# Optimization experiments

Hardware: AMD Instinct MI355X
Metric: run time of the kernel (lower is better)

The kernel has to match this reference:

```python
import jax, jax.numpy as jnp
import numpy as np

N, E, D, L, V = 200000, 500000, 128, 5, 8
BN_EPS = 1e-5


def _bn(h, g, b, m, v):
    # eval-mode BatchNorm1d with running stats
    return (h - m) * jax.lax.rsqrt(v + BN_EPS) * g + b


def setup_inputs() -> dict:
    key = jax.random.key(0)
    ks = iter(jax.random.split(key, 40))
    nk = lambda: next(ks)
    f = lambda shape: jax.random.normal(nk(), shape, jnp.float32) * 0.05
    inp = {}
    inp["x"] = jax.random.normal(nk(), (N, 12), jnp.float32)
    inp["edge_index"] = jax.random.randint(nk(), (2, E), 0, N, dtype=jnp.int32)
    inp["edge_attr"] = jax.random.randint(nk(), (E, 3), 0, V, dtype=jnp.int32)
    # atom encoder: Lin(12,D) -> BN -> ReLU -> Lin(D,D) -> BN -> ReLU -> Lin(D,D)
    inp["ae_W1"] = f((12, D)); inp["ae_b1"] = jnp.zeros((D,), jnp.float32)
    inp["ae_g1"] = jnp.ones((D,), jnp.float32); inp["ae_be1"] = jnp.zeros((D,), jnp.float32)
    inp["ae_m1"] = f((D,)); inp["ae_v1"] = jax.random.uniform(nk(), (D,), jnp.float32) + 0.5
    inp["ae_W2"] = f((D, D)); inp["ae_b2"] = jnp.zeros((D,), jnp.float32)
    inp["ae_g2"] = jnp.ones((D,), jnp.float32); inp["ae_be2"] = jnp.zeros((D,), jnp.float32)
    inp["ae_m2"] = f((D,)); inp["ae_v2"] = jax.random.uniform(nk(), (D,), jnp.float32) + 0.5
    inp["ae_W3"] = f((D, D)); inp["ae_b3"] = jnp.zeros((D,), jnp.float32)
    # per-layer GIN params (stacked over L)
    inp["bond_emb"] = f((L, 3, V, D))
    inp["eps"] = jnp.zeros((L,), jnp.float32)
    inp["mlp_W1"] = f((L, D, D)); inp["mlp_b1"] = jnp.zeros((L, D), jnp.float32)
    inp["mlp_g"] = jnp.ones((L, D), jnp.float32); inp["mlp_be"] = jnp.zeros((L, D), jnp.float32)
    inp["mlp_m"] = f((L, D)); inp["mlp_v"] = jax.random.uniform(nk(), (L, D), jnp.float32) + 0.5
    inp["mlp_W2"] = f((L, D, D)); inp["mlp_b2"] = jnp.zeros((L, D), jnp.float32)
    # per-layer outer BatchNorm
    inp["out_g"] = jnp.ones((L, D), jnp.float32); inp["out_be"] = jnp.zeros((L, D), jnp.float32)
    inp["out_m"] = f((L, D)); inp["out_v"] = jax.random.uniform(nk(), (L, D), jnp.float32) + 0.5
    return inp


def reference(x, edge_index, edge_attr,
              ae_W1, ae_b1, ae_g1, ae_be1, ae_m1, ae_v1,
              ae_W2, ae_b2, ae_g2, ae_be2, ae_m2, ae_v2,
              ae_W3, ae_b3,
              bond_emb, eps, mlp_W1, mlp_b1, mlp_g, mlp_be, mlp_m, mlp_v,
              mlp_W2, mlp_b2, out_g, out_be, out_m, out_v):
    n_nodes = x.shape[0]
    src, dst = edge_index[0], edge_index[1]
    # atom encoder
    h = jax.nn.relu(_bn(x @ ae_W1 + ae_b1, ae_g1, ae_be1, ae_m1, ae_v1))
    h = jax.nn.relu(_bn(h @ ae_W2 + ae_b2, ae_g2, ae_be2, ae_m2, ae_v2))
    h = h @ ae_W3 + ae_b3  # [N, D]
    n_layers = bond_emb.shape[0]
    for l in range(n_layers):
        # BondEncoder: sum of per-feature embeddings -> [E, D]
        be = bond_emb[l]
        e_emb = be[0][edge_attr[:, 0]] + be[1][edge_attr[:, 1]] + be[2][edge_attr[:, 2]]
        # message: relu(x_j + edge_emb); aggregate: scatter-add at dst
        msg = jax.nn.relu(h[src] + e_emb)
        agg = jax.ops.segment_sum(msg, dst, num_segments=n_nodes)
        z = (1.0 + eps[l]) * h + agg
        # GIN MLP: Lin -> BN -> ReLU -> Lin
        z = jax.nn.relu(_bn(z @ mlp_W1[l] + mlp_b1[l], mlp_g[l], mlp_be[l], mlp_m[l], mlp_v[l]))
        z = z @ mlp_W2[l] + mlp_b2[l]
        # outer BatchNorm; ReLU on all but last layer (dropout is identity in eval)
        z = _bn(z, out_g[l], out_be[l], out_m[l], out_v[l])
        if l < n_layers - 1:
            z = jax.nn.relu(z)
        h = z
    return h  # JK='last'
```

## Files before the change

### kernel.cpp

```cpp
#include <hip/hip_runtime.h>
#include <hip/hip_bf16.h>
#include <cstdint>
#include <cstddef>

#define D 128
#define NNODES 200000
#define NEDGES 500000
#define NLAYERS 5
#define BN_EPS 1e-5f
#define MAXDEG 24

typedef __attribute__((ext_vector_type(8))) short bf16x8;
typedef __attribute__((ext_vector_type(4))) float f32x4;

__device__ __forceinline__ unsigned short f2bf(float f) {
    union { float f; unsigned int u; } x; x.f = f;
    unsigned int r = (x.u + 0x7FFFu + ((x.u >> 16) & 1u)) >> 16;
    return (unsigned short)r;
}
__device__ __forceinline__ float bf2f(unsigned short u) {
    union { unsigned int u; float f; } x; x.u = ((unsigned int)u) << 16; return x.f;
}

__global__ void k_zero(int* __restrict__ p, int n) {
    int i = blockIdx.x * 256 + threadIdx.x;
    if (i < n) p[i] = 0;
}

__global__ void k_fill_edges(const int* __restrict__ ei, const int* __restrict__ ea,
                             int* __restrict__ deg, int* __restrict__ elist, int n_edges) {
    int e = blockIdx.x * 256 + threadIdx.x;
    if (e >= n_edges) return;
    int dst = ei[n_edges + e];
    int src = ei[e];
    int a0 = ea[e * 3], a1 = ea[e * 3 + 1], a2 = ea[e * 3 + 2];
    int rec = src | (a0 << 18) | (a1 << 21) | (a2 << 24);
    int pos = atomicAdd(&deg[dst], 1);
    if (pos < MAXDEG) elist[dst * MAXDEG + pos] = rec;
}

__global__ void k_prep_w(const float* __restrict__ aeW2, const float* __restrict__ aeW3,
                         const float* __restrict__ mlpW1, const float* __restrict__ mlpW2,
                         unsigned short* __restrict__ wbt) {
    int m = blockIdx.x >> 3;
    int s = (blockIdx.x & 7) * 256 + threadIdx.x;
    int f = s >> 4;
    int kc = (s & 15) * 8;
    const float* W;
    if (m == 0) W = aeW2;
    else if (m == 1) W = aeW3;
    else if (m < 7) W = mlpW1 + (size_t)(m - 2) * D * D;
    else W = mlpW2 + (size_t)(m - 7) * D * D;
    unsigned short tmp[8];
#pragma unroll
    for (int j = 0; j < 8; ++j) tmp[j] = f2bf(W[(size_t)(kc + j) * D + f]);
    *(int4*)(wbt + (size_t)m * D * D + (size_t)f * D + kc) = *(int4*)tmp;
}

__global__ void k_bondsum(const float* __restrict__ bond, float* __restrict__ bsum) {
    int idx = blockIdx.x;
    int l = idx >> 9, combo = idx & 511;
    int a0 = combo & 7, a1 = (combo >> 3) & 7, a2 = (combo >> 6) & 7;
    int f = threadIdx.x;
    const float* bl = bond + (size_t)l * 3 * 8 * 128;
    bsum[(size_t)idx * 128 + f] =
        bl[a0 * 128 + f] + bl[1024 + a1 * 128 + f] + bl[2048 + a2 * 128 + f];
}

__global__ void k_ae1(const float* __restrict__ x, const float* __restrict__ W,
                      const float* __restrict__ b, const float* __restrict__ g,
                      const float* __restrict__ be, const float* __restrict__ m,
                      const float* __restrict__ v, unsigned short* __restrict__ out) {
    __shared__ float sW[12][128];
    int tid = threadIdx.x;
    for (int i = tid; i < 12 * 128; i += 256) sW[i >> 7][i & 127] = W[i];
    int f0 = (tid & 31) * 4;
    int g8 = tid >> 5;
    float4 bb = *(const float4*)(b + f0);
    float4 gg = *(const float4*)(g + f0);
    float4 ee = *(const float4*)(be + f0);
    float4 mm = *(const float4*)(m + f0);
    float4 vv = *(const float4*)(v + f0);
    float A0 = gg.x * rsqrtf(vv.x + BN_EPS), S0 = (bb.x - mm.x) * A0 + ee.x;
    float A1 = gg.y * rsqrtf(vv.y + BN_EPS), S1 = (bb.y - mm.y) * A1 + ee.y;
    float A2 = gg.z * rsqrtf(vv.z + BN_EPS), S2 = (bb.z - mm.z) * A2 + ee.z;
    float A3 = gg.w * rsqrtf(vv.w + BN_EPS), S3 = (bb.w - mm.w) * A3 + ee.w;
    __syncthreads();
    for (int n = blockIdx.x * 8 + g8; n < NNODES; n += gridDim.x * 8) {
        const float4* xr = (const float4*)(x + (size_t)n * 12);
        float4 x0 = xr[0], x1 = xr[1], x2 = xr[2];
        float xv[12] = {x0.x, x0.y, x0.z, x0.w, x1.x, x1.y, x1.z, x1.w,
                        x2.x, x2.y, x2.z, x2.w};
        float a0 = 0.f, a1 = 0.f, a2 = 0.f, a3 = 0.f;
#pragma unroll
        for (int k = 0; k < 12; ++k) {
            float4 wv = *(float4*)&sW[k][f0];
            a0 += xv[k] * wv.x; a1 += xv[k] * wv.y;
            a2 += xv[k] * wv.z; a3 += xv[k] * wv.w;
        }
        unsigned short o[4];
        o[0] = f2bf(fmaxf(a0 * A0 + S0, 0.f));
        o[1] = f2bf(fmaxf(a1 * A1 + S1, 0.f));
        o[2] = f2bf(fmaxf(a2 * A2 + S2, 0.f));
        o[3] = f2bf(fmaxf(a3 * A3 + S3, 0.f));
        *(uint2*)(out + (size_t)n * D + f0) = *(uint2*)o;
    }
}

__launch_bounds__(256, 7)
__global__ void k_agg(const unsigned short* __restrict__ hin,
                      const float* __restrict__ bsum,
                      const float* __restrict__ eps_arr, int layer,
                      const int* __restrict__ deg, const int* __restrict__ elist,
                      unsigned short* __restrict__ out) {
    int tid = threadIdx.x;
    int f4 = tid & 31;
    int n = blockIdx.x * 8 + (tid >> 5);
    int dgr = min(deg[n], MAXDEG);
    int rec = (f4 < MAXDEG) ? elist[(size_t)n * MAXDEG + f4] : 0;
    float epsv = 1.f + eps_arr[layer];
    ushort4 hs = *(const ushort4*)(hin + (size_t)n * D + f4 * 4);
    float z0 = epsv * bf2f(hs.x), z1 = epsv * bf2f(hs.y);
    float z2 = epsv * bf2f(hs.z), z3 = epsv * bf2f(hs.w);

    ushort4 hv[6]; float4 bv[6]; int rr[6];
#pragma unroll
    for (int j = 0; j < 6; ++j) {
        rr[j] = __shfl(rec, j, 32);
        if (j < dgr) {
            hv[j] = *(const ushort4*)(hin + (size_t)(rr[j] & 0x3FFFF) * D + f4 * 4);
            bv[j] = *(const float4*)(bsum + (size_t)((rr[j] >> 18) & 511) * D + f4 * 4);
        }
    }
#pragma unroll
    for (int j = 0; j < 6; ++j) {
        if (j < dgr) {
            z0 += fmaxf(bf2f(hv[j].x) + bv[j].x, 0.f);
            z1 += fmaxf(bf2f(hv[j].y) + bv[j].y, 0.f);
            z2 += fmaxf(bf2f(hv[j].z) + bv[j].z, 0.f);
            z3 += fmaxf(bf2f(hv[j].w) + bv[j].w, 0.f);
        }
    }
    for (int base = 6; base < dgr; base += 4) {
        ushort4 hw[4]; float4 bw[4]; int rt[4];
#pragma unroll
        for (int j = 0; j < 4; ++j) {
            rt[j] = __shfl(rec, base + j, 32);
            if (base + j < dgr) {
                hw[j] = *(const ushort4*)(hin + (size_t)(rt[j] & 0x3FFFF) * D + f4 * 4);
                bw[j] = *(const float4*)(bsum + (size_t)((rt[j] >> 18) & 511) * D + f4 * 4);
            }
        }
#pragma unroll
        for (int j = 0; j < 4; ++j) {
            if (base + j < dgr) {
                z0 += fmaxf(bf2f(hw[j].x) + bw[j].x, 0.f);
                z1 += fmaxf(bf2f(hw[j].y) + bw[j].y, 0.f);
                z2 += fmaxf(bf2f(hw[j].z) + bw[j].z, 0.f);
                z3 += fmaxf(bf2f(hw[j].w) + bw[j].w, 0.f);
            }
        }
    }
    unsigned short o[4] = {f2bf(z0), f2bf(z1), f2bf(z2), f2bf(z3)};
    *(uint2*)(out + (size_t)n * D + f4 * 4) = *(uint2*)o;
}

#define SWZ(row, bytecol) (((row) * 256 + (bytecol)) ^ (((row) & 7) << 4))
template<int OUTF32>
__launch_bounds__(512, 6)
__global__ void k_mlp2(const unsigned short* __restrict__ hin,
                       const unsigned short* __restrict__ W1t,
                       const float* __restrict__ b1,
                       const float* __restrict__ g1, const float* __restrict__ be1,
                       const float* __restrict__ m1, const float* __restrict__ v1,
                       const unsigned short* __restrict__ W2t,
                       const float* __restrict__ b2,
                       const float* __restrict__ g2, const float* __restrict__ be2,
                       const float* __restrict__ m2, const float* __restrict__ v2,
                       unsigned short* __restrict__ outb, float* __restrict__ outf,
                       int do_bn2, int do_relu2) {
    __shared__ char sA[16384];
    int tid = threadIdx.x;
    size_t nb = (size_t)blockIdx.x * 64;
    int lane = tid & 63;
    int w = tid >> 6;
    int arow = lane & 15;
    int kq = (lane >> 4) * 8;
    int c = w * 16 + arow;

    bf16x8 w1f[4], w2f[4];
#pragma unroll
    for (int kb = 0; kb < 4; ++kb) {
        w1f[kb] = *(const bf16x8*)(W1t + (size_t)c * D + kb * 32 + kq);
        w2f[kb] = *(const bf16x8*)(W2t + (size_t)c * D + kb * 32 + kq);
    }
#pragma unroll
    for (int i = 0; i < 2; ++i) {
        int s = tid + i * 512;
        int r = s >> 4, cc = (s & 15) * 16;
        *(int4*)(sA + SWZ(r, cc)) = *(const int4*)((const char*)hin + (nb + r) * 256 + cc);
    }
    __syncthreads();

    f32x4 acc[4];
#pragma unroll
    for (int rt = 0; rt < 4; ++rt) acc[rt] = (f32x4){0.f, 0.f, 0.f, 0.f};
#pragma unroll
    for (int kb = 0; kb < 4; ++kb) {
        int k0 = kb * 32 + kq;
#pragma unroll
        for (int rt = 0; rt < 4; ++rt) {
            bf16x8 a = *(bf16x8*)(sA + SWZ(rt * 16 + arow, k0 * 2));
            acc[rt] = __builtin_amdgcn_mfma_f32_16x16x32_bf16(a, w1f[kb], acc[rt], 0, 0, 0);
        }
    }
    __syncthreads();

    {
        float sc = g1[c] * rsqrtf(v1[c] + BN_EPS);
        float sh = (b1[c] - m1[c]) * sc + be1[c];
#pragma unroll
        for (int rt = 0; rt < 4; ++rt) {
#pragma unroll
            for (int r = 0; r < 4; ++r) {
                int row = rt * 16 + (lane >> 4) * 4 + r;
                float z = fmaxf(acc[rt][r] * sc + sh, 0.f);
                *(unsigned short*)(sA + SWZ(row, c * 2)) = f2bf(z);
            }
        }
    }
    __syncthreads();

#pragma unroll
    for (int rt = 0; rt < 4; ++rt) acc[rt] = (f32x4){0.f, 0.f, 0.f, 0.f};
#pragma unroll
    for (int kb = 0; kb < 4; ++kb) {
        int k0 = kb * 32 + kq;
#pragma unroll
        for (int rt = 0; rt < 4; ++rt) {
            bf16x8 a = *(bf16x8*)(sA + SWZ(rt * 16 + arow, k0 * 2));
            acc[rt] = __builtin_amdgcn_mfma_f32_16x16x32_bf16(a, w2f[kb], acc[rt], 0, 0, 0);
        }
    }

    float sc2 = 1.f, sh2;
    if (do_bn2) { sc2 = g2[c] * rsqrtf(v2[c] + BN_EPS); sh2 = (b2[c] - m2[c]) * sc2 + be2[c]; }
    else sh2 = b2[c];
    if constexpr (OUTF32) {
#pragma unroll
        for (int rt = 0; rt < 4; ++rt) {
#pragma unroll
            for (int r = 0; r < 4; ++r) {
                int row = rt * 16 + (lane >> 4) * 4 + r;
                float z = acc[rt][r] * sc2 + sh2;
                if (do_relu2) z = fmaxf(z, 0.f);
                outf[(nb + row) * D + c] = z;
            }
        }
    } else {
        __syncthreads();
#pragma unroll
        for (int rt = 0; rt < 4; ++rt) {
#pragma unroll
            for (int r = 0; r < 4; ++r) {
                int row = rt * 16 + (lane >> 4) * 4 + r;
                float z = acc[rt][r] * sc2 + sh2;
                if (do_relu2) z = fmaxf(z, 0.f);
                *(unsigned short*)(sA + SWZ(row, c * 2)) = f2bf(z);
            }
        }
        __syncthreads();
#pragma unroll
        for (int i = 0; i < 2; ++i) {
            int s = tid + i * 512;
            int r = s >> 4, cc = (s & 15) * 16;
            *(int4*)((char*)outb + (nb + r) * 256 + cc) = *(int4*)(sA + SWZ(r, cc));
        }
    }
}

extern "C" void kernel_launch(void* const* d_in, const int* in_sizes, int n_in,
                              void* d_out, int out_size, void* d_ws, size_t ws_size,
                              hipStream_t stream) {
    const float* x      = (const float*)d_in[0];
    const int*   ei     = (const int*)d_in[1];
    const int*   ea     = (const int*)d_in[2];
    const float* aeW1   = (const float*)d_in[3];
    const float* aeb1   = (const float*)d_in[4];
    const float* aeg1   = (const float*)d_in[5];
    const float* aebe1  = (const float*)d_in[6];
    const float* aem1   = (const float*)d_in[7];
    const float* aev1   = (const float*)d_in[8];
    const float* aeW2   = (const float*)d_in[9];
    const float* aeb2   = (const float*)d_in[10];
    const float* aeg2   = (const float*)d_in[11];
    const float* aebe2  = (const float*)d_in[12];
    const float* aem2   = (const float*)d_in[13];
    const float* aev2   = (const float*)d_in[14];
    const float* aeW3   = (const float*)d_in[15];
    const float* aeb3   = (const float*)d_in[16];
    const float* bond   = (const float*)d_in[17];
    const float* eps    = (const float*)d_in[18];
    const float* mlpW1  = (const float*)d_in[19];
    const float* mlpb1  = (const float*)d_in[20];
    const float* mlpg   = (const float*)d_in[21];
    const float* mlpbe  = (const float*)d_in[22];
    const float* mlpm   = (const float*)d_in[23];
    const float* mlpv   = (const float*)d_in[24];
    const float* mlpW2  = (const float*)d_in[25];
    const float* mlpb2  = (const float*)d_in[26];
    const float* outg   = (const float*)d_in[27];
    const float* outbe  = (const float*)d_in[28];
    const float* outm   = (const float*)d_in[29];
    const float* outv   = (const float*)d_in[30];

    char* ws = (char*)d_ws;
    unsigned short* hA  = (unsigned short*)ws;
    unsigned short* hB  = (unsigned short*)(ws + 51200000);
    int*   deg   = (int*)(ws + 102400000);
    int*   elist = (int*)(ws + 103200000);
    unsigned short* wbt = (unsigned short*)(ws + 122400000);
    float* bsum  = (float*)(ws + 122793216);
    float* outF = (float*)d_out;

    k_zero<<<(NNODES + 255) / 256, 256, 0, stream>>>(deg, NNODES);
    k_fill_edges<<<(NEDGES + 255) / 256, 256, 0, stream>>>(ei, ea, deg, elist, NEDGES);
    k_prep_w<<<96, 256, 0, stream>>>(aeW2, aeW3, mlpW1, mlpW2, wbt);
    k_bondsum<<<NLAYERS * 512, 128, 0, stream>>>(bond, bsum);

    k_ae1<<<1280, 256, 0, stream>>>(x, aeW1, aeb1, aeg1, aebe1, aem1, aev1, hA);
    dim3 gg(NNODES / 64);
    k_mlp2<0><<<gg, 512, 0, stream>>>(hA,
        wbt + 0 * 16384, aeb2, aeg2, aebe2, aem2, aev2,
        wbt + 1 * 16384, aeb3, aeb3, aeb3, aeb3, aeb3,
        hB, nullptr, 0, 0);

    unsigned short* hc = hB;
    for (int l = 0; l < NLAYERS; ++l) {
        unsigned short* ho = (hc == hB) ? hA : hB;
        const unsigned short* W1 = wbt + (size_t)(2 + l) * 16384;
        const unsigned short* W2 = wbt + (size_t)(7 + l) * 16384;
        k_agg<<<NNODES / 8, 256, 0, stream>>>(hc, bsum + (size_t)l * 512 * 128,
                                              eps, l, deg, elist, ho);
        if (l < NLAYERS - 1) {
            k_mlp2<0><<<gg, 512, 0, stream>>>(ho,
                W1, mlpb1 + (size_t)l * D, mlpg + (size_t)l * D, mlpbe + (size_t)l * D,
                mlpm + (size_t)l * D, mlpv + (size_t)l * D,
                W2, mlpb2 + (size_t)l * D, outg + (size_t)l * D, outbe + (size_t)l * D,
                outm + (size_t)l * D, outv + (size_t)l * D,
                ho, nullptr, 1, 1);
            hc = ho;
        } else {
            k_mlp2<1><<<gg, 512, 0, stream>>>(ho,
                W1, mlpb1 + (size_t)l * D, mlpg + (size_t)l * D, mlpbe + (size_t)l * D,
                mlpm + (size_t)l * D, mlpv + (size_t)l * D,
                W2, mlpb2 + (size_t)l * D, outg + (size_t)l * D, outbe + (size_t)l * D,
                outm + (size_t)l * D, outv + (size_t)l * D,
                nullptr, outF, 1, 0);
        }
    }
    (void)in_sizes; (void)n_in; (void)out_size; (void)ws_size;
}
```

Before: 481.5 us.

## Store bond-sum table in bf16 and double-buffer MLP LDS to drop barriers

The precomputed bond-embedding sum table is now stored as bf16 instead of fp32, which halves the bytes each edge gather reads in the aggregation kernel. The aggregation kernel's occupancy hint rises from 7 to 8 blocks per CU. The fused MLP kernel gets a second 16KB shared buffer for the hidden activations, so two __syncthreads between the first GEMM and the LDS writes can be removed. In exchange, edge embeddings lose precision, and the MLP kernel uses more LDS per block, which may lower its occupancy.

```diff
diff --git a/kernel.cpp b/kernel.cpp
--- a/kernel.cpp
+++ b/kernel.cpp
@@ -57,14 +57,14 @@
     *(int4*)(wbt + (size_t)m * D * D + (size_t)f * D + kc) = *(int4*)tmp;
 }
 
-__global__ void k_bondsum(const float* __restrict__ bond, float* __restrict__ bsum) {
+__global__ void k_bondsum(const float* __restrict__ bond, unsigned short* __restrict__ bsum) {
     int idx = blockIdx.x;
     int l = idx >> 9, combo = idx & 511;
     int a0 = combo & 7, a1 = (combo >> 3) & 7, a2 = (combo >> 6) & 7;
     int f = threadIdx.x;
     const float* bl = bond + (size_t)l * 3 * 8 * 128;
     bsum[(size_t)idx * 128 + f] =
-        bl[a0 * 128 + f] + bl[1024 + a1 * 128 + f] + bl[2048 + a2 * 128 + f];
+        f2bf(bl[a0 * 128 + f] + bl[1024 + a1 * 128 + f] + bl[2048 + a2 * 128 + f]);
 }
 
 __global__ void k_ae1(const float* __restrict__ x, const float* __restrict__ W,
@@ -107,9 +107,9 @@
     }
 }
 
-__launch_bounds__(256, 7)
+__launch_bounds__(256, 8)
 __global__ void k_agg(const unsigned short* __restrict__ hin,
-                      const float* __restrict__ bsum,
+                      const unsigned short* __restrict__ bsum,
                       const float* __restrict__ eps_arr, int layer,
                       const int* __restrict__ deg, const int* __restrict__ elist,
                       unsigned short* __restrict__ out) {
@@ -123,41 +123,41 @@
     float z0 = epsv * bf2f(hs.x), z1 = epsv * bf2f(hs.y);
     float z2 = epsv * bf2f(hs.z), z3 = epsv * bf2f(hs.w);
 
-    ushort4 hv[6]; float4 bv[6]; int rr[6];
+    ushort4 hv[6]; ushort4 bv[6]; int rr[6];
 #pragma unroll
     for (int j = 0; j < 6; ++j) {
         rr[j] = __shfl(rec, j, 32);
         if (j < dgr) {
             hv[j] = *(const ushort4*)(hin + (size_t)(rr[j] & 0x3FFFF) * D + f4 * 4);
-            bv[j] = *(const float4*)(bsum + (size_t)((rr[j] >> 18) & 511) * D + f4 * 4);
+            bv[j] = *(const ushort4*)(bsum + (size_t)((rr[j] >> 18) & 511) * D + f4 * 4);
         }
     }
 #pragma unroll
     for (int j = 0; j < 6; ++j) {
         if (j < dgr) {
-            z0 += fmaxf(bf2f(hv[j].x) + bv[j].x, 0.f);
-            z1 += fmaxf(bf2f(hv[j].y) + bv[j].y, 0.f);
-            z2 += fmaxf(bf2f(hv[j].z) + bv[j].z, 0.f);
-            z3 += fmaxf(bf2f(hv[j].w) + bv[j].w, 0.f);
+            z0 += fmaxf(bf2f(hv[j].x) + bf2f(bv[j].x), 0.f);
+            z1 += fmaxf(bf2f(hv[j].y) + bf2f(bv[j].y), 0.f);
+            z2 += fmaxf(bf2f(hv[j].z) + bf2f(bv[j].z), 0.f);
+            z3 += fmaxf(bf2f(hv[j].w) + bf2f(bv[j].w), 0.f);
         }
     }
     for (int base = 6; base < dgr; base += 4) {
-        ushort4 hw[4]; float4 bw[4]; int rt[4];
+        ushort4 hw[4]; ushort4 bw[4]; int rt[4];
 #pragma unroll
         for (int j = 0; j < 4; ++j) {
             rt[j] = __shfl(rec, base + j, 32);
             if (base + j < dgr) {
                 hw[j] = *(const ushort4*)(hin + (size_t)(rt[j] & 0x3FFFF) * D + f4 * 4);
-                bw[j] = *(const float4*)(bsum + (size_t)((rt[j] >> 18) & 511) * D + f4 * 4);
+                bw[j] = *(const ushort4*)(bsum + (size_t)((rt[j] >> 18) & 511) * D + f4 * 4);
             }
         }
 #pragma unroll
         for (int j = 0; j < 4; ++j) {
             if (base + j < dgr) {
-                z0 += fmaxf(bf2f(hw[j].x) + bw[j].x, 0.f);
-                z1 += fmaxf(bf2f(hw[j].y) + bw[j].y, 0.f);
-                z2 += fmaxf(bf2f(hw[j].z) + bw[j].z, 0.f);
-                z3 += fmaxf(bf2f(hw[j].w) + bw[j].w, 0.f);
+                z0 += fmaxf(bf2f(hw[j].x) + bf2f(bw[j].x), 0.f);
+                z1 += fmaxf(bf2f(hw[j].y) + bf2f(bw[j].y), 0.f);
+                z2 += fmaxf(bf2f(hw[j].z) + bf2f(bw[j].z), 0.f);
+                z3 += fmaxf(bf2f(hw[j].w) + bf2f(bw[j].w), 0.f);
             }
         }
     }
@@ -180,6 +180,7 @@
                        unsigned short* __restrict__ outb, float* __restrict__ outf,
                        int do_bn2, int do_relu2) {
     __shared__ char sA[16384];
+    __shared__ char sZ[16384];
     int tid = threadIdx.x;
     size_t nb = (size_t)blockIdx.x * 64;
     int lane = tid & 63;
@@ -214,7 +215,6 @@
             acc[rt] = __builtin_amdgcn_mfma_f32_16x16x32_bf16(a, w1f[kb], acc[rt], 0, 0, 0);
         }
     }
-    __syncthreads();
 
     {
         float sc = g1[c] * rsqrtf(v1[c] + BN_EPS);
@@ -225,7 +225,7 @@
             for (int r = 0; r < 4; ++r) {
                 int row = rt * 16 + (lane >> 4) * 4 + r;
                 float z = fmaxf(acc[rt][r] * sc + sh, 0.f);
-                *(unsigned short*)(sA + SWZ(row, c * 2)) = f2bf(z);
+                *(unsigned short*)(sZ + SWZ(row, c * 2)) = f2bf(z);
             }
         }
     }
@@ -238,7 +238,7 @@
         int k0 = kb * 32 + kq;
 #pragma unroll
         for (int rt = 0; rt < 4; ++rt) {
-            bf16x8 a = *(bf16x8*)(sA + SWZ(rt * 16 + arow, k0 * 2));
+            bf16x8 a = *(bf16x8*)(sZ + SWZ(rt * 16 + arow, k0 * 2));
             acc[rt] = __builtin_amdgcn_mfma_f32_16x16x32_bf16(a, w2f[kb], acc[rt], 0, 0, 0);
         }
     }
@@ -258,7 +258,6 @@
             }
         }
     } else {
-        __syncthreads();
 #pragma unroll
         for (int rt = 0; rt < 4; ++rt) {
 #pragma unroll
@@ -320,7 +319,7 @@
     int*   deg   = (int*)(ws + 102400000);
     int*   elist = (int*)(ws + 103200000);
     unsigned short* wbt = (unsigned short*)(ws + 122400000);
-    float* bsum  = (float*)(ws + 122793216);
+    unsigned short* bsum = (unsigned short*)(ws + 122793216);
     float* outF = (float*)d_out;
 
     k_zero<<<(NNODES + 255) / 256, 256, 0, stream>>>(deg, NNODES);
```

Measured after the change: 484.0 us. About the same (+0.5%).
